# Optimization experiments

Measured on AMD Instinct MI355X. Metric: run time of the kernel, lower is better.

Reference implementation:

```python
import jax, jax.numpy as jnp
import numpy as np

B, S, D, H = 2, 2048, 2048, 16
HD = D // H  # head_dim = 128
ROPE_BASE = 10000.0


def _rope_tables(seq_len, head_dim, base, dtype):
    inv_freq = 1.0 / (base ** (jnp.arange(0, head_dim, 2, dtype=jnp.float32) / head_dim))
    t = jnp.arange(seq_len, dtype=jnp.float32)
    freqs = jnp.einsum('s,d->sd', t, inv_freq)           # [S, HD/2]
    emb = jnp.concatenate([freqs, freqs], axis=-1)        # [S, HD]
    return jnp.cos(emb).astype(dtype), jnp.sin(emb).astype(dtype)


def _rotate_half(x):
    half = x.shape[-1] // 2
    return jnp.concatenate([-x[..., half:], x[..., :half]], axis=-1)


def setup_inputs() -> dict:
    key = jax.random.key(0)
    kx, kq, kk, kv, ko = jax.random.split(key, 5)
    std = 0.02
    return {
        'x': jax.random.normal(kx, (B, S, D), dtype=jnp.float32),
        'Wq': jax.random.normal(kq, (D, D), dtype=jnp.float32) * std,
        'Wk': jax.random.normal(kk, (D, D), dtype=jnp.float32) * std,
        'Wv': jax.random.normal(kv, (D, D), dtype=jnp.float32) * std,
        'Wo': jax.random.normal(ko, (D, D), dtype=jnp.float32) * std,
    }


def reference(x, Wq, Wk, Wv, Wo):
    b, s, d = x.shape
    scale = HD ** -0.5
    # projections (nn.Linear: x @ W.T), split heads -> [b, h, s, hd]
    q = (x @ Wq.T).reshape(b, s, H, HD).transpose(0, 2, 1, 3)
    k = (x @ Wk.T).reshape(b, s, H, HD).transpose(0, 2, 1, 3)
    v = (x @ Wv.T).reshape(b, s, H, HD).transpose(0, 2, 1, 3)
    cos, sin = _rope_tables(s, HD, ROPE_BASE, x.dtype)    # [s, hd]
    q = q * cos + _rotate_half(q) * sin
    k = k * cos + _rotate_half(k) * sin
    scores = jnp.einsum('bhqd,bhkd->bhqk', q, k) * scale  # [b,h,s,s]
    causal = jnp.triu(jnp.ones((s, s), dtype=bool), k=1)
    scores = jnp.where(causal, jnp.float32(-jnp.inf).astype(scores.dtype), scores)
    attn = jax.nn.softmax(scores, axis=-1)
    out = jnp.einsum('bhqk,bhkd->bhqd', attn, v)
    out = out.transpose(0, 2, 1, 3).reshape(b, s, d)
    return out @ Wo.T
```

## Files before the change

### kernel.cpp

```cpp
#include <hip/hip_runtime.h>
#include <hip/hip_bf16.h>
#include <cstdint>
#include <cstddef>

#define B_ 2
#define S_ 2048
#define D_ 2048
#define H_ 16
#define HD_ 128

typedef __bf16 bf16_t;
typedef __bf16 bf16x8 __attribute__((ext_vector_type(8)));
typedef __bf16 bf16x4 __attribute__((ext_vector_type(4)));
typedef short s16x4 __attribute__((ext_vector_type(4)));
typedef float f32x4 __attribute__((ext_vector_type(4)));

__device__ __forceinline__ void async16(const bf16_t* g, bf16_t* l) {
    __builtin_amdgcn_global_load_lds(
        (const __attribute__((address_space(1))) unsigned int*)g,
        (__attribute__((address_space(3))) unsigned int*)l, 16, 0, 0);
}

__device__ __forceinline__ f32x4 mfma16x16x16_bf16(bf16x4 a, bf16x4 b, f32x4 c) {
#if __has_builtin(__builtin_amdgcn_mfma_f32_16x16x16_bf16)
    return __builtin_amdgcn_mfma_f32_16x16x16_bf16(a, b, c, 0, 0, 0);
#elif __has_builtin(__builtin_amdgcn_mfma_f32_16x16x16bf16_1k)
    return __builtin_amdgcn_mfma_f32_16x16x16bf16_1k(
        __builtin_bit_cast(s16x4, a), __builtin_bit_cast(s16x4, b), c, 0, 0, 0);
#else
    f32x4 d = c;
    asm("v_mfma_f32_16x16x16_bf16 %0, %1, %2, %0" : "+v"(d) : "v"(a), "v"(b));
    return d;
#endif
}

__global__ void f2b_multi(const float* __restrict__ x, const float* __restrict__ wq,
                          const float* __restrict__ wk, const float* __restrict__ wv,
                          const float* __restrict__ wo, bf16_t* __restrict__ xb,
                          bf16_t* __restrict__ wqb, bf16_t* __restrict__ wkb,
                          bf16_t* __restrict__ wvb, bf16_t* __restrict__ wob) {
    const float* in; bf16_t* out;
    switch (blockIdx.y) {
        case 0: in = x;            out = xb;            break;
        case 1: in = x + 4194304;  out = xb + 4194304;  break;
        case 2: in = wq;           out = wqb;           break;
        case 3: in = wk;           out = wkb;           break;
        case 4: in = wv;           out = wvb;           break;
        default: in = wo;          out = wob;           break;
    }
    int i = (blockIdx.x * blockDim.x + threadIdx.x) * 4;
    float4 v = *(const float4*)(in + i);
    bf16x4 o = { (bf16_t)v.x, (bf16_t)v.y, (bf16_t)v.z, (bf16_t)v.w };
    *(bf16x4*)(out + i) = o;
}

__global__ void rope_kernel(bf16_t* __restrict__ q, bf16_t* __restrict__ k) {
    int idx = blockIdx.x * blockDim.x + threadIdx.x;
    bf16_t* p = (blockIdx.y == 0) ? q : k;
    float sc = (blockIdx.y == 0) ? 0.08838834764831845f : 1.0f;
    int i0 = (idx & 7) * 8;
    int rest = idx >> 3;
    int h = rest & (H_ - 1);
    int row = rest >> 4;
    int s = row & (S_ - 1);
    size_t base = (size_t)row * D_ + (size_t)h * HD_ + i0;
    bf16x8 x0 = *(bf16x8*)(p + base);
    bf16x8 x1 = *(bf16x8*)(p + base + 64);
    bf16x8 o0, o1;
#pragma unroll
    for (int j = 0; j < 8; ++j) {
        float inv = __expf(-(float)(i0 + j) * 0.14391156831212787f);
        float ang = (float)s * inv;
        float sn, c;
        __sincosf(ang, &sn, &c);
        sn *= sc; c *= sc;
        float a = (float)x0[j], bb = (float)x1[j];
        o0[j] = (bf16_t)(a * c - bb * sn);
        o1[j] = (bf16_t)(bb * c + a * sn);
    }
    *(bf16x8*)(p + base) = o0;
    *(bf16x8*)(p + base + 64) = o1;
}

__global__ __launch_bounds__(256) void gemm_qkv(const bf16_t* __restrict__ A,
                                                const bf16_t* __restrict__ Wq,
                                                const bf16_t* __restrict__ Wk,
                                                const bf16_t* __restrict__ Wv,
                                                bf16_t* __restrict__ qb,
                                                bf16_t* __restrict__ kb,
                                                bf16_t* __restrict__ vtb) {
    __shared__ __align__(16) bf16_t As[128 * 32];
    __shared__ __align__(16) bf16_t Bs[128 * 32];
    const int K = D_;
    int t = threadIdx.x;
    int w = t >> 6, lane = t & 63, lo = lane & 15, hi = lane >> 4;
    int seg = blockIdx.x >> 4;
    int n0 = (blockIdx.x & 15) * 128;
    int m0 = blockIdx.y * 128;
    const bf16_t* Bt = (seg == 0) ? Wq : (seg == 1) ? Wk : Wv;
    int wm = (w & 1) * 64, wn = (w >> 1) * 64;
    f32x4 acc[4][4] = {};
    const bf16_t* ga = A + (size_t)(m0 + (t >> 2)) * K + (t & 3) * 8;
    const bf16_t* gb = Bt + (size_t)(n0 + (t >> 2)) * K + (t & 3) * 8;
    for (int k0 = 0; k0 < K; k0 += 32) {
        async16(ga + k0,                  As + t * 8);
        async16(ga + (size_t)64 * K + k0, As + 2048 + t * 8);
        async16(gb + k0,                  Bs + t * 8);
        async16(gb + (size_t)64 * K + k0, Bs + 2048 + t * 8);
        __syncthreads();
        bf16x8 af[4], bfr[4];
#pragma unroll
        for (int ms = 0; ms < 4; ++ms)
            af[ms] = *(const bf16x8*)(As + (wm + ms * 16 + lo) * 32 + hi * 8);
#pragma unroll
        for (int ns = 0; ns < 4; ++ns)
            bfr[ns] = *(const bf16x8*)(Bs + (wn + ns * 16 + lo) * 32 + hi * 8);
#pragma unroll
        for (int ms = 0; ms < 4; ++ms)
#pragma unroll
            for (int ns = 0; ns < 4; ++ns)
                acc[ms][ns] = __builtin_amdgcn_mfma_f32_16x16x32_bf16(af[ms], bfr[ns], acc[ms][ns], 0, 0, 0);
        __syncthreads();
    }
    if (seg < 2) {
        bf16_t* C = (seg == 0) ? qb : kb;
#pragma unroll
        for (int ms = 0; ms < 4; ++ms)
#pragma unroll
            for (int ns = 0; ns < 4; ++ns)
#pragma unroll
                for (int r = 0; r < 4; ++r)
                    C[(size_t)(m0 + wm + ms * 16 + hi * 4 + r) * D_ + n0 + wn + ns * 16 + lo] = (bf16_t)acc[ms][ns][r];
    } else {
#pragma unroll
        for (int ms = 0; ms < 4; ++ms) {
            int mrow = m0 + wm + ms * 16 + hi * 4;
            int bb = mrow >> 11, s = mrow & (S_ - 1);
#pragma unroll
            for (int ns = 0; ns < 4; ++ns) {
                int d = n0 + wn + ns * 16 + lo;
                bf16x4 pv = { (bf16_t)acc[ms][ns][0], (bf16_t)acc[ms][ns][1],
                              (bf16_t)acc[ms][ns][2], (bf16_t)acc[ms][ns][3] };
                *(bf16x4*)(vtb + (size_t)bb * D_ * S_ + (size_t)d * S_ + s) = pv;
            }
        }
    }
}

__global__ __launch_bounds__(256) void gemm_bt_f32(const bf16_t* __restrict__ A,
                                                   const bf16_t* __restrict__ Bt,
                                                   float* __restrict__ C,
                                                   int M, int N, int K) {
    __shared__ __align__(16) bf16_t As[128 * 32];
    __shared__ __align__(16) bf16_t Bs[128 * 32];
    int t = threadIdx.x;
    int w = t >> 6, lane = t & 63, lo = lane & 15, hi = lane >> 4;
    int m0 = blockIdx.y * 128, n0 = blockIdx.x * 128;
    int wm = (w & 1) * 64, wn = (w >> 1) * 64;
    f32x4 acc[4][4] = {};
    const bf16_t* ga = A + (size_t)(m0 + (t >> 2)) * K + (t & 3) * 8;
    const bf16_t* gb = Bt + (size_t)(n0 + (t >> 2)) * K + (t & 3) * 8;
    for (int k0 = 0; k0 < K; k0 += 32) {
        async16(ga + k0,                  As + t * 8);
        async16(ga + (size_t)64 * K + k0, As + 2048 + t * 8);
        async16(gb + k0,                  Bs + t * 8);
        async16(gb + (size_t)64 * K + k0, Bs + 2048 + t * 8);
        __syncthreads();
        bf16x8 af[4], bfr[4];
#pragma unroll
        for (int ms = 0; ms < 4; ++ms)
            af[ms] = *(const bf16x8*)(As + (wm + ms * 16 + lo) * 32 + hi * 8);
#pragma unroll
        for (int ns = 0; ns < 4; ++ns)
            bfr[ns] = *(const bf16x8*)(Bs + (wn + ns * 16 + lo) * 32 + hi * 8);
#pragma unroll
        for (int ms = 0; ms < 4; ++ms)
#pragma unroll
            for (int ns = 0; ns < 4; ++ns)
                acc[ms][ns] = __builtin_amdgcn_mfma_f32_16x16x32_bf16(af[ms], bfr[ns], acc[ms][ns], 0, 0, 0);
        __syncthreads();
    }
#pragma unroll
    for (int ms = 0; ms < 4; ++ms)
#pragma unroll
        for (int ns = 0; ns < 4; ++ns)
#pragma unroll
            for (int r = 0; r < 4; ++r)
                C[(size_t)(m0 + wm + ms * 16 + hi * 4 + r) * N + n0 + wn + ns * 16 + lo] = acc[ms][ns][r];
}

__global__ __launch_bounds__(256) void attn_kernel(const bf16_t* __restrict__ q,
                                                   const bf16_t* __restrict__ k,
                                                   const bf16_t* __restrict__ vt,
                                                   bf16_t* __restrict__ o) {
    __shared__ __align__(16) bf16_t Ks[64 * 128];
    __shared__ __align__(16) bf16_t Vs[128 * 64];
    int t = threadIdx.x;
    int w = t >> 6, lane = t & 63, lo = lane & 15, hi = lane >> 4;
    int bx = blockIdx.x;
    int b = blockIdx.y >> 4, h = blockIdx.y & 15;
    const size_t head_off = (size_t)b * S_ * D_ + (size_t)h * HD_;
    const size_t vhead_off = ((size_t)b * D_ + (size_t)h * HD_) * S_;

#pragma unroll 1
    for (int pass = 0; pass < 2; ++pass) {
        int qt = pass ? (31 - bx) : bx;
        int q0 = qt * 64;
        int qg = q0 + w * 16 + lo;
        bf16x8 aq[4];
#pragma unroll
        for (int c = 0; c < 4; ++c)
            aq[c] = *(const bf16x8*)(q + head_off + (size_t)qg * D_ + c * 32 + hi * 8);

        float l_part = 0.f;
        f32x4 oacc[8] = {};
        int nkt = qt + 1;
        for (int kt = 0; kt < nkt; ++kt) {
            int k0 = kt * 64;
            __syncthreads();
#pragma unroll
            for (int i = 0; i < 4; ++i) {
                int chunk = w * 4 + i;
                int r = chunk * 4 + (lane >> 4);
                int lc = (lane & 15) ^ (r & 15);
                async16(k + head_off + (size_t)(k0 + r) * D_ + lc * 8,
                        Ks + chunk * 512 + lane * 8);
            }
#pragma unroll
            for (int i = 0; i < 4; ++i) {
                int chunk = w * 4 + i;
                int d = chunk * 8 + (lane >> 3);
                int lc = (lane & 7) ^ (d & 7);
                async16(vt + vhead_off + (size_t)d * S_ + k0 + lc * 8,
                        Vs + chunk * 512 + lane * 8);
            }
            __syncthreads();

            f32x4 sacc[4] = {};
#pragma unroll
            for (int c = 0; c < 4; ++c) {
#pragma unroll
                for (int nt = 0; nt < 4; ++nt) {
                    int row = nt * 16 + lo;
                    int pc = (c * 4 + hi) ^ lo;
                    bf16x8 ak = *(const bf16x8*)(Ks + row * 128 + pc * 8);
                    sacc[nt] = __builtin_amdgcn_mfma_f32_16x16x32_bf16(ak, aq[c], sacc[nt], 0, 0, 0);
                }
            }
            bool diag = (kt == qt);
            bf16x4 pf[4];
#pragma unroll
            for (int nt = 0; nt < 4; ++nt) {
#pragma unroll
                for (int r = 0; r < 4; ++r) {
                    float e = __expf(fminf(sacc[nt][r], 60.f));
                    if (diag) {
                        int kg = k0 + nt * 16 + hi * 4 + r;
                        if (kg > qg) e = 0.f;
                    }
                    l_part += e;
                    pf[nt][r] = (bf16_t)e;
                }
            }
#pragma unroll
            for (int nt = 0; nt < 4; ++nt) {
                int kkb = nt * 16 + hi * 4;
                int chunk8 = kkb >> 3, rem = kkb & 7;
#pragma unroll
                for (int dt = 0; dt < 8; ++dt) {
                    int d = dt * 16 + lo;
                    bf16x4 av = *(const bf16x4*)(Vs + d * 64 + (chunk8 ^ (d & 7)) * 8 + rem);
                    oacc[dt] = mfma16x16x16_bf16(av, pf[nt], oacc[dt]);
                }
            }
        }
        float l = l_part;
        l += __shfl_xor(l, 16);
        l += __shfl_xor(l, 32);
        float rl = 1.0f / l;
#pragma unroll
        for (int dt = 0; dt < 8; ++dt) {
            bf16x4 ov = { (bf16_t)(oacc[dt][0] * rl), (bf16_t)(oacc[dt][1] * rl),
                          (bf16_t)(oacc[dt][2] * rl), (bf16_t)(oacc[dt][3] * rl) };
            *(bf16x4*)(o + head_off + (size_t)qg * D_ + dt * 16 + hi * 4) = ov;
        }
    }
}

extern "C" void kernel_launch(void* const* d_in, const int* in_sizes, int n_in,
                              void* d_out, int out_size, void* d_ws, size_t ws_size,
                              hipStream_t stream) {
    (void)in_sizes; (void)n_in; (void)out_size; (void)ws_size;
    const float* x  = (const float*)d_in[0];
    const float* Wq = (const float*)d_in[1];
    const float* Wk = (const float*)d_in[2];
    const float* Wv = (const float*)d_in[3];
    const float* Wo = (const float*)d_in[4];
    char* ws = (char*)d_ws;
    bf16_t* xb  = (bf16_t*)(ws);
    bf16_t* Wqb = (bf16_t*)(ws + 16777216);
    bf16_t* Wkb = (bf16_t*)(ws + 25165824);
    bf16_t* Wvb = (bf16_t*)(ws + 33554432);
    bf16_t* Wob = (bf16_t*)(ws + 41943040);
    bf16_t* qb  = (bf16_t*)(ws + 50331648);
    bf16_t* kb  = (bf16_t*)(ws + 67108864);
    bf16_t* vtb = (bf16_t*)(ws + 83886080);
    bf16_t* ob  = (bf16_t*)(ws + 100663296);
    float* out = (float*)d_out;

    f2b_multi<<<dim3(4096, 6), 256, 0, stream>>>(x, Wq, Wk, Wv, Wo, xb, Wqb, Wkb, Wvb, Wob);

    gemm_qkv<<<dim3(48, 32), 256, 0, stream>>>(xb, Wqb, Wkb, Wvb, qb, kb, vtb);

    rope_kernel<<<dim3((B_ * S_ * H_ * 8) / 256, 2), 256, 0, stream>>>(qb, kb);

    attn_kernel<<<dim3(16, B_ * H_), 256, 0, stream>>>(qb, kb, vtb, ob);

    gemm_bt_f32<<<dim3(D_ / 128, (B_ * S_) / 128), 256, 0, stream>>>(ob, Wob, out, B_ * S_, D_, D_);
}
```

Measured before the change: 407.9 us.

## Fuse RoPE into QKV GEMM epilogue and enlarge attention key tiles to 128

A precomputed cos/sin table replaces the standalone RoPE kernel. Rotation now happens in the QKV GEMM epilogue, with wave N-columns remapped so each lane holds both rotation halves. The softmax scale is folded into the Wq bf16 conversion. The attention kernel processes 128-key tiles with larger shared-memory buffers and skips waves fully past the causal boundary, trading an extra memory pass for higher LDS use and possible occupancy loss.

```diff
diff --git a/kernel.cpp b/kernel.cpp
--- a/kernel.cpp
+++ b/kernel.cpp
@@ -40,52 +40,36 @@
                           bf16_t* __restrict__ wqb, bf16_t* __restrict__ wkb,
                           bf16_t* __restrict__ wvb, bf16_t* __restrict__ wob) {
     const float* in; bf16_t* out;
+    float sc = 1.0f;
     switch (blockIdx.y) {
         case 0: in = x;            out = xb;            break;
         case 1: in = x + 4194304;  out = xb + 4194304;  break;
-        case 2: in = wq;           out = wqb;           break;
+        case 2: in = wq;           out = wqb; sc = 0.08838834764831845f; break;
         case 3: in = wk;           out = wkb;           break;
         case 4: in = wv;           out = wvb;           break;
         default: in = wo;          out = wob;           break;
     }
     int i = (blockIdx.x * blockDim.x + threadIdx.x) * 4;
     float4 v = *(const float4*)(in + i);
-    bf16x4 o = { (bf16_t)v.x, (bf16_t)v.y, (bf16_t)v.z, (bf16_t)v.w };
+    bf16x4 o = { (bf16_t)(v.x * sc), (bf16_t)(v.y * sc), (bf16_t)(v.z * sc), (bf16_t)(v.w * sc) };
     *(bf16x4*)(out + i) = o;
 }
 
-__global__ void rope_kernel(bf16_t* __restrict__ q, bf16_t* __restrict__ k) {
+__global__ void rope_tab(float2* __restrict__ tab) {
     int idx = blockIdx.x * blockDim.x + threadIdx.x;
-    bf16_t* p = (blockIdx.y == 0) ? q : k;
-    float sc = (blockIdx.y == 0) ? 0.08838834764831845f : 1.0f;
-    int i0 = (idx & 7) * 8;
-    int rest = idx >> 3;
-    int h = rest & (H_ - 1);
-    int row = rest >> 4;
-    int s = row & (S_ - 1);
-    size_t base = (size_t)row * D_ + (size_t)h * HD_ + i0;
-    bf16x8 x0 = *(bf16x8*)(p + base);
-    bf16x8 x1 = *(bf16x8*)(p + base + 64);
-    bf16x8 o0, o1;
-#pragma unroll
-    for (int j = 0; j < 8; ++j) {
-        float inv = __expf(-(float)(i0 + j) * 0.14391156831212787f);
-        float ang = (float)s * inv;
-        float sn, c;
-        __sincosf(ang, &sn, &c);
-        sn *= sc; c *= sc;
-        float a = (float)x0[j], bb = (float)x1[j];
-        o0[j] = (bf16_t)(a * c - bb * sn);
-        o1[j] = (bf16_t)(bb * c + a * sn);
-    }
-    *(bf16x8*)(p + base) = o0;
-    *(bf16x8*)(p + base + 64) = o1;
+    int s = idx >> 6, j = idx & 63;
+    float inv = __expf(-(float)j * 0.14391156831212787f);
+    float ang = (float)s * inv;
+    float sn, c;
+    __sincosf(ang, &sn, &c);
+    tab[idx] = make_float2(c, sn);
 }
 
 __global__ __launch_bounds__(256) void gemm_qkv(const bf16_t* __restrict__ A,
                                                 const bf16_t* __restrict__ Wq,
                                                 const bf16_t* __restrict__ Wk,
                                                 const bf16_t* __restrict__ Wv,
+                                                const float2* __restrict__ tab,
                                                 bf16_t* __restrict__ qb,
                                                 bf16_t* __restrict__ kb,
                                                 bf16_t* __restrict__ vtb) {
@@ -98,7 +82,7 @@
     int n0 = (blockIdx.x & 15) * 128;
     int m0 = blockIdx.y * 128;
     const bf16_t* Bt = (seg == 0) ? Wq : (seg == 1) ? Wk : Wv;
-    int wm = (w & 1) * 64, wn = (w >> 1) * 64;
+    int wm = (w & 1) * 64, W = (w >> 1);
     f32x4 acc[4][4] = {};
     const bf16_t* ga = A + (size_t)(m0 + (t >> 2)) * K + (t & 3) * 8;
     const bf16_t* gb = Bt + (size_t)(n0 + (t >> 2)) * K + (t & 3) * 8;
@@ -114,7 +98,7 @@
             af[ms] = *(const bf16x8*)(As + (wm + ms * 16 + lo) * 32 + hi * 8);
 #pragma unroll
         for (int ns = 0; ns < 4; ++ns)
-            bfr[ns] = *(const bf16x8*)(Bs + (wn + ns * 16 + lo) * 32 + hi * 8);
+            bfr[ns] = *(const bf16x8*)(Bs + (W * 16 + ns * 32 + lo) * 32 + hi * 8);
 #pragma unroll
         for (int ms = 0; ms < 4; ++ms)
 #pragma unroll
@@ -124,13 +108,25 @@
     }
     if (seg < 2) {
         bf16_t* C = (seg == 0) ? qb : kb;
-#pragma unroll
-        for (int ms = 0; ms < 4; ++ms)
-#pragma unroll
-            for (int ns = 0; ns < 4; ++ns)
-#pragma unroll
-                for (int r = 0; r < 4; ++r)
-                    C[(size_t)(m0 + wm + ms * 16 + hi * 4 + r) * D_ + n0 + wn + ns * 16 + lo] = (bf16_t)acc[ms][ns][r];
+        int j0 = W * 16 + lo;
+#pragma unroll
+        for (int ms = 0; ms < 4; ++ms) {
+            int mbase = m0 + wm + ms * 16 + hi * 4;
+#pragma unroll
+            for (int r = 0; r < 4; ++r) {
+                int m = mbase + r;
+                int s = m & (S_ - 1);
+                const float2* trow = tab + s * 64;
+#pragma unroll
+                for (int ns = 0; ns < 2; ++ns) {
+                    int j = j0 + ns * 32;
+                    float2 cs = trow[j];
+                    float v0 = acc[ms][ns][r], v1 = acc[ms][ns + 2][r];
+                    C[(size_t)m * D_ + n0 + j]      = (bf16_t)(v0 * cs.x - v1 * cs.y);
+                    C[(size_t)m * D_ + n0 + j + 64] = (bf16_t)(v1 * cs.x + v0 * cs.y);
+                }
+            }
+        }
     } else {
 #pragma unroll
         for (int ms = 0; ms < 4; ++ms) {
@@ -138,7 +134,7 @@
             int bb = mrow >> 11, s = mrow & (S_ - 1);
 #pragma unroll
             for (int ns = 0; ns < 4; ++ns) {
-                int d = n0 + wn + ns * 16 + lo;
+                int d = n0 + W * 16 + ns * 32 + lo;
                 bf16x4 pv = { (bf16_t)acc[ms][ns][0], (bf16_t)acc[ms][ns][1],
                               (bf16_t)acc[ms][ns][2], (bf16_t)acc[ms][ns][3] };
                 *(bf16x4*)(vtb + (size_t)bb * D_ * S_ + (size_t)d * S_ + s) = pv;
@@ -193,8 +189,8 @@
                                                    const bf16_t* __restrict__ k,
                                                    const bf16_t* __restrict__ vt,
                                                    bf16_t* __restrict__ o) {
-    __shared__ __align__(16) bf16_t Ks[64 * 128];
-    __shared__ __align__(16) bf16_t Vs[128 * 64];
+    __shared__ __align__(16) bf16_t Ks[128 * 128];
+    __shared__ __align__(16) bf16_t Vs[128 * 128];
     int t = threadIdx.x;
     int w = t >> 6, lane = t & 63, lo = lane & 15, hi = lane >> 4;
     int bx = blockIdx.x;
@@ -214,63 +210,65 @@
 
         float l_part = 0.f;
         f32x4 oacc[8] = {};
-        int nkt = qt + 1;
+        int nkt = (qt >> 1) + 1;
         for (int kt = 0; kt < nkt; ++kt) {
-            int k0 = kt * 64;
+            int k0 = kt * 128;
             __syncthreads();
 #pragma unroll
-            for (int i = 0; i < 4; ++i) {
-                int chunk = w * 4 + i;
+            for (int i = 0; i < 8; ++i) {
+                int chunk = w * 8 + i;
                 int r = chunk * 4 + (lane >> 4);
                 int lc = (lane & 15) ^ (r & 15);
                 async16(k + head_off + (size_t)(k0 + r) * D_ + lc * 8,
                         Ks + chunk * 512 + lane * 8);
             }
 #pragma unroll
-            for (int i = 0; i < 4; ++i) {
-                int chunk = w * 4 + i;
-                int d = chunk * 8 + (lane >> 3);
-                int lc = (lane & 7) ^ (d & 7);
+            for (int i = 0; i < 8; ++i) {
+                int chunk = w * 8 + i;
+                int d = chunk * 4 + (lane >> 4);
+                int lc = (lane & 15) ^ (d & 15);
                 async16(vt + vhead_off + (size_t)d * S_ + k0 + lc * 8,
                         Vs + chunk * 512 + lane * 8);
             }
             __syncthreads();
 
-            f32x4 sacc[4] = {};
-#pragma unroll
-            for (int c = 0; c < 4; ++c) {
-#pragma unroll
-                for (int nt = 0; nt < 4; ++nt) {
-                    int row = nt * 16 + lo;
-                    int pc = (c * 4 + hi) ^ lo;
-                    bf16x8 ak = *(const bf16x8*)(Ks + row * 128 + pc * 8);
-                    sacc[nt] = __builtin_amdgcn_mfma_f32_16x16x32_bf16(ak, aq[c], sacc[nt], 0, 0, 0);
+            if (k0 <= q0 + w * 16 + 15) {
+                f32x4 sacc[8] = {};
+#pragma unroll
+                for (int c = 0; c < 4; ++c) {
+#pragma unroll
+                    for (int nt = 0; nt < 8; ++nt) {
+                        int row = nt * 16 + lo;
+                        int pc = (c * 4 + hi) ^ lo;
+                        bf16x8 ak = *(const bf16x8*)(Ks + row * 128 + pc * 8);
+                        sacc[nt] = __builtin_amdgcn_mfma_f32_16x16x32_bf16(ak, aq[c], sacc[nt], 0, 0, 0);
+                    }
                 }
-            }
-            bool diag = (kt == qt);
-            bf16x4 pf[4];
-#pragma unroll
-            for (int nt = 0; nt < 4; ++nt) {
-#pragma unroll
-                for (int r = 0; r < 4; ++r) {
-                    float e = __expf(fminf(sacc[nt][r], 60.f));
-                    if (diag) {
-                        int kg = k0 + nt * 16 + hi * 4 + r;
-                        if (kg > qg) e = 0.f;
+                bool diag = (k0 + 127 > q0 + w * 16);
+                bf16x4 pf[8];
+#pragma unroll
+                for (int nt = 0; nt < 8; ++nt) {
+#pragma unroll
+                    for (int r = 0; r < 4; ++r) {
+                        float e = __expf(fminf(sacc[nt][r], 60.f));
+                        if (diag) {
+                            int kg = k0 + nt * 16 + hi * 4 + r;
+                            if (kg > qg) e = 0.f;
+                        }
+                        l_part += e;
+                        pf[nt][r] = (bf16_t)e;
                     }
-                    l_part += e;
-                    pf[nt][r] = (bf16_t)e;
                 }
-            }
-#pragma unroll
-            for (int nt = 0; nt < 4; ++nt) {
-                int kkb = nt * 16 + hi * 4;
-                int chunk8 = kkb >> 3, rem = kkb & 7;
-#pragma unroll
-                for (int dt = 0; dt < 8; ++dt) {
-                    int d = dt * 16 + lo;
-                    bf16x4 av = *(const bf16x4*)(Vs + d * 64 + (chunk8 ^ (d & 7)) * 8 + rem);
-                    oacc[dt] = mfma16x16x16_bf16(av, pf[nt], oacc[dt]);
+#pragma unroll
+                for (int nt = 0; nt < 8; ++nt) {
+                    int kkb = nt * 16 + hi * 4;
+                    int c16 = kkb >> 3, rem = kkb & 7;
+#pragma unroll
+                    for (int dt = 0; dt < 8; ++dt) {
+                        int d = dt * 16 + lo;
+                        bf16x4 av = *(const bf16x4*)(Vs + d * 128 + (c16 ^ (d & 15)) * 8 + rem);
+                        oacc[dt] = mfma16x16x16_bf16(av, pf[nt], oacc[dt]);
+                    }
                 }
             }
         }
@@ -306,13 +304,13 @@
     bf16_t* kb  = (bf16_t*)(ws + 67108864);
     bf16_t* vtb = (bf16_t*)(ws + 83886080);
     bf16_t* ob  = (bf16_t*)(ws + 100663296);
+    float2* tab = (float2*)(ws + 100663296);
     float* out = (float*)d_out;
 
+    rope_tab<<<512, 256, 0, stream>>>(tab);
     f2b_multi<<<dim3(4096, 6), 256, 0, stream>>>(x, Wq, Wk, Wv, Wo, xb, Wqb, Wkb, Wvb, Wob);
 
-    gemm_qkv<<<dim3(48, 32), 256, 0, stream>>>(xb, Wqb, Wkb, Wvb, qb, kb, vtb);
-
-    rope_kernel<<<dim3((B_ * S_ * H_ * 8) / 256, 2), 256, 0, stream>>>(qb, kb);
+    gemm_qkv<<<dim3(48, 32), 256, 0, stream>>>(xb, Wqb, Wkb, Wvb, tab, qb, kb, vtb);
 
     attn_kernel<<<dim3(16, B_ * H_), 256, 0, stream>>>(qb, kb, vtb, ob);
 
```

Result: slower. 419.0 us (+2.7%).

## Widen GEMM K-tile to 64 with swizzled LDS and use 128-key attention tiles

Applied to the files above, without the earlier changes.

Both GEMM kernels now stage a 64-wide K slice per iteration with an XOR-swizzled LDS layout, which halves the number of barrier pairs per tile and is meant to reduce LDS bank conflicts. The attention kernel loads 128 keys per iteration instead of 64, and each wave skips tiles that lie entirely above its causal boundary. The softmax scale is folded into the Wq conversion instead of the RoPE kernel. These changes raise LDS use and register pressure (attention LDS doubles to 64KB), which can lower occupancy.

```diff
diff --git a/kernel.cpp b/kernel.cpp
--- a/kernel.cpp
+++ b/kernel.cpp
@@ -40,24 +40,24 @@
                           bf16_t* __restrict__ wqb, bf16_t* __restrict__ wkb,
                           bf16_t* __restrict__ wvb, bf16_t* __restrict__ wob) {
     const float* in; bf16_t* out;
+    float sc = 1.0f;
     switch (blockIdx.y) {
         case 0: in = x;            out = xb;            break;
         case 1: in = x + 4194304;  out = xb + 4194304;  break;
-        case 2: in = wq;           out = wqb;           break;
+        case 2: in = wq;           out = wqb; sc = 0.08838834764831845f; break;
         case 3: in = wk;           out = wkb;           break;
         case 4: in = wv;           out = wvb;           break;
         default: in = wo;          out = wob;           break;
     }
     int i = (blockIdx.x * blockDim.x + threadIdx.x) * 4;
     float4 v = *(const float4*)(in + i);
-    bf16x4 o = { (bf16_t)v.x, (bf16_t)v.y, (bf16_t)v.z, (bf16_t)v.w };
+    bf16x4 o = { (bf16_t)(v.x * sc), (bf16_t)(v.y * sc), (bf16_t)(v.z * sc), (bf16_t)(v.w * sc) };
     *(bf16x4*)(out + i) = o;
 }
 
 __global__ void rope_kernel(bf16_t* __restrict__ q, bf16_t* __restrict__ k) {
     int idx = blockIdx.x * blockDim.x + threadIdx.x;
     bf16_t* p = (blockIdx.y == 0) ? q : k;
-    float sc = (blockIdx.y == 0) ? 0.08838834764831845f : 1.0f;
     int i0 = (idx & 7) * 8;
     int rest = idx >> 3;
     int h = rest & (H_ - 1);
@@ -73,7 +73,6 @@
         float ang = (float)s * inv;
         float sn, c;
         __sincosf(ang, &sn, &c);
-        sn *= sc; c *= sc;
         float a = (float)x0[j], bb = (float)x1[j];
         o0[j] = (bf16_t)(a * c - bb * sn);
         o1[j] = (bf16_t)(bb * c + a * sn);
@@ -81,6 +80,7 @@
     *(bf16x8*)(p + base) = o0;
     *(bf16x8*)(p + base + 64) = o1;
 }
+
 
 __global__ __launch_bounds__(256) void gemm_qkv(const bf16_t* __restrict__ A,
                                                 const bf16_t* __restrict__ Wq,
@@ -89,8 +89,8 @@
                                                 bf16_t* __restrict__ qb,
                                                 bf16_t* __restrict__ kb,
                                                 bf16_t* __restrict__ vtb) {
-    __shared__ __align__(16) bf16_t As[128 * 32];
-    __shared__ __align__(16) bf16_t Bs[128 * 32];
+    __shared__ __align__(16) bf16_t As[128 * 64];
+    __shared__ __align__(16) bf16_t Bs[128 * 64];
     const int K = D_;
     int t = threadIdx.x;
     int w = t >> 6, lane = t & 63, lo = lane & 15, hi = lane >> 4;
@@ -100,26 +100,35 @@
     const bf16_t* Bt = (seg == 0) ? Wq : (seg == 1) ? Wk : Wv;
     int wm = (w & 1) * 64, wn = (w >> 1) * 64;
     f32x4 acc[4][4] = {};
-    const bf16_t* ga = A + (size_t)(m0 + (t >> 2)) * K + (t & 3) * 8;
-    const bf16_t* gb = Bt + (size_t)(n0 + (t >> 2)) * K + (t & 3) * 8;
-    for (int k0 = 0; k0 < K; k0 += 32) {
-        async16(ga + k0,                  As + t * 8);
-        async16(ga + (size_t)64 * K + k0, As + 2048 + t * 8);
-        async16(gb + k0,                  Bs + t * 8);
-        async16(gb + (size_t)64 * K + k0, Bs + 2048 + t * 8);
+    int srow = w * 32 + (lane >> 3);
+    int scol = ((lane & 7) ^ (lane >> 3)) * 8;
+    const bf16_t* gA = A  + (size_t)(m0 + srow) * K + scol;
+    const bf16_t* gB = Bt + (size_t)(n0 + srow) * K + scol;
+    bf16_t* lA = As + w * 2048 + lane * 8;
+    bf16_t* lB = Bs + w * 2048 + lane * 8;
+    for (int k0 = 0; k0 < K; k0 += 64) {
+#pragma unroll
+        for (int i = 0; i < 4; ++i) {
+            async16(gA + (size_t)(i * 8) * K + k0, lA + i * 512);
+            async16(gB + (size_t)(i * 8) * K + k0, lB + i * 512);
+        }
         __syncthreads();
-        bf16x8 af[4], bfr[4];
-#pragma unroll
-        for (int ms = 0; ms < 4; ++ms)
-            af[ms] = *(const bf16x8*)(As + (wm + ms * 16 + lo) * 32 + hi * 8);
-#pragma unroll
-        for (int ns = 0; ns < 4; ++ns)
-            bfr[ns] = *(const bf16x8*)(Bs + (wn + ns * 16 + lo) * 32 + hi * 8);
-#pragma unroll
-        for (int ms = 0; ms < 4; ++ms)
+#pragma unroll
+        for (int kk = 0; kk < 2; ++kk) {
+            bf16x8 af[4], bfr[4];
+            int pc = (kk * 4 + hi) ^ (lo & 7);
+#pragma unroll
+            for (int ms = 0; ms < 4; ++ms)
+                af[ms] = *(const bf16x8*)(As + (wm + ms * 16 + lo) * 64 + pc * 8);
 #pragma unroll
             for (int ns = 0; ns < 4; ++ns)
-                acc[ms][ns] = __builtin_amdgcn_mfma_f32_16x16x32_bf16(af[ms], bfr[ns], acc[ms][ns], 0, 0, 0);
+                bfr[ns] = *(const bf16x8*)(Bs + (wn + ns * 16 + lo) * 64 + pc * 8);
+#pragma unroll
+            for (int ms = 0; ms < 4; ++ms)
+#pragma unroll
+                for (int ns = 0; ns < 4; ++ns)
+                    acc[ms][ns] = __builtin_amdgcn_mfma_f32_16x16x32_bf16(af[ms], bfr[ns], acc[ms][ns], 0, 0, 0);
+        }
         __syncthreads();
     }
     if (seg < 2) {
@@ -151,33 +160,42 @@
                                                    const bf16_t* __restrict__ Bt,
                                                    float* __restrict__ C,
                                                    int M, int N, int K) {
-    __shared__ __align__(16) bf16_t As[128 * 32];
-    __shared__ __align__(16) bf16_t Bs[128 * 32];
+    __shared__ __align__(16) bf16_t As[128 * 64];
+    __shared__ __align__(16) bf16_t Bs[128 * 64];
     int t = threadIdx.x;
     int w = t >> 6, lane = t & 63, lo = lane & 15, hi = lane >> 4;
     int m0 = blockIdx.y * 128, n0 = blockIdx.x * 128;
     int wm = (w & 1) * 64, wn = (w >> 1) * 64;
     f32x4 acc[4][4] = {};
-    const bf16_t* ga = A + (size_t)(m0 + (t >> 2)) * K + (t & 3) * 8;
-    const bf16_t* gb = Bt + (size_t)(n0 + (t >> 2)) * K + (t & 3) * 8;
-    for (int k0 = 0; k0 < K; k0 += 32) {
-        async16(ga + k0,                  As + t * 8);
-        async16(ga + (size_t)64 * K + k0, As + 2048 + t * 8);
-        async16(gb + k0,                  Bs + t * 8);
-        async16(gb + (size_t)64 * K + k0, Bs + 2048 + t * 8);
+    int srow = w * 32 + (lane >> 3);
+    int scol = ((lane & 7) ^ (lane >> 3)) * 8;
+    const bf16_t* gA = A  + (size_t)(m0 + srow) * K + scol;
+    const bf16_t* gB = Bt + (size_t)(n0 + srow) * K + scol;
+    bf16_t* lA = As + w * 2048 + lane * 8;
+    bf16_t* lB = Bs + w * 2048 + lane * 8;
+    for (int k0 = 0; k0 < K; k0 += 64) {
+#pragma unroll
+        for (int i = 0; i < 4; ++i) {
+            async16(gA + (size_t)(i * 8) * K + k0, lA + i * 512);
+            async16(gB + (size_t)(i * 8) * K + k0, lB + i * 512);
+        }
         __syncthreads();
-        bf16x8 af[4], bfr[4];
-#pragma unroll
-        for (int ms = 0; ms < 4; ++ms)
-            af[ms] = *(const bf16x8*)(As + (wm + ms * 16 + lo) * 32 + hi * 8);
-#pragma unroll
-        for (int ns = 0; ns < 4; ++ns)
-            bfr[ns] = *(const bf16x8*)(Bs + (wn + ns * 16 + lo) * 32 + hi * 8);
-#pragma unroll
-        for (int ms = 0; ms < 4; ++ms)
+#pragma unroll
+        for (int kk = 0; kk < 2; ++kk) {
+            bf16x8 af[4], bfr[4];
+            int pc = (kk * 4 + hi) ^ (lo & 7);
+#pragma unroll
+            for (int ms = 0; ms < 4; ++ms)
+                af[ms] = *(const bf16x8*)(As + (wm + ms * 16 + lo) * 64 + pc * 8);
 #pragma unroll
             for (int ns = 0; ns < 4; ++ns)
-                acc[ms][ns] = __builtin_amdgcn_mfma_f32_16x16x32_bf16(af[ms], bfr[ns], acc[ms][ns], 0, 0, 0);
+                bfr[ns] = *(const bf16x8*)(Bs + (wn + ns * 16 + lo) * 64 + pc * 8);
+#pragma unroll
+            for (int ms = 0; ms < 4; ++ms)
+#pragma unroll
+                for (int ns = 0; ns < 4; ++ns)
+                    acc[ms][ns] = __builtin_amdgcn_mfma_f32_16x16x32_bf16(af[ms], bfr[ns], acc[ms][ns], 0, 0, 0);
+        }
         __syncthreads();
     }
 #pragma unroll
@@ -193,8 +211,8 @@
                                                    const bf16_t* __restrict__ k,
                                                    const bf16_t* __restrict__ vt,
                                                    bf16_t* __restrict__ o) {
-    __shared__ __align__(16) bf16_t Ks[64 * 128];
-    __shared__ __align__(16) bf16_t Vs[128 * 64];
+    __shared__ __align__(16) bf16_t Ks[128 * 128];
+    __shared__ __align__(16) bf16_t Vs[128 * 128];
     int t = threadIdx.x;
     int w = t >> 6, lane = t & 63, lo = lane & 15, hi = lane >> 4;
     int bx = blockIdx.x;
@@ -214,63 +232,65 @@
 
         float l_part = 0.f;
         f32x4 oacc[8] = {};
-        int nkt = qt + 1;
+        int nkt = (qt >> 1) + 1;
         for (int kt = 0; kt < nkt; ++kt) {
-            int k0 = kt * 64;
+            int k0 = kt * 128;
             __syncthreads();
 #pragma unroll
-            for (int i = 0; i < 4; ++i) {
-                int chunk = w * 4 + i;
+            for (int i = 0; i < 8; ++i) {
+                int chunk = w * 8 + i;
                 int r = chunk * 4 + (lane >> 4);
                 int lc = (lane & 15) ^ (r & 15);
                 async16(k + head_off + (size_t)(k0 + r) * D_ + lc * 8,
                         Ks + chunk * 512 + lane * 8);
             }
 #pragma unroll
-            for (int i = 0; i < 4; ++i) {
-                int chunk = w * 4 + i;
-                int d = chunk * 8 + (lane >> 3);
-                int lc = (lane & 7) ^ (d & 7);
+            for (int i = 0; i < 8; ++i) {
+                int chunk = w * 8 + i;
+                int d = chunk * 4 + (lane >> 4);
+                int lc = (lane & 15) ^ (d & 15);
                 async16(vt + vhead_off + (size_t)d * S_ + k0 + lc * 8,
                         Vs + chunk * 512 + lane * 8);
             }
             __syncthreads();
 
-            f32x4 sacc[4] = {};
-#pragma unroll
-            for (int c = 0; c < 4; ++c) {
-#pragma unroll
-                for (int nt = 0; nt < 4; ++nt) {
-                    int row = nt * 16 + lo;
-                    int pc = (c * 4 + hi) ^ lo;
-                    bf16x8 ak = *(const bf16x8*)(Ks + row * 128 + pc * 8);
-                    sacc[nt] = __builtin_amdgcn_mfma_f32_16x16x32_bf16(ak, aq[c], sacc[nt], 0, 0, 0);
+            if (k0 <= q0 + w * 16 + 15) {
+                f32x4 sacc[8] = {};
+#pragma unroll
+                for (int c = 0; c < 4; ++c) {
+#pragma unroll
+                    for (int nt = 0; nt < 8; ++nt) {
+                        int row = nt * 16 + lo;
+                        int pc = (c * 4 + hi) ^ lo;
+                        bf16x8 ak = *(const bf16x8*)(Ks + row * 128 + pc * 8);
+                        sacc[nt] = __builtin_amdgcn_mfma_f32_16x16x32_bf16(ak, aq[c], sacc[nt], 0, 0, 0);
+                    }
                 }
-            }
-            bool diag = (kt == qt);
-            bf16x4 pf[4];
-#pragma unroll
-            for (int nt = 0; nt < 4; ++nt) {
-#pragma unroll
-                for (int r = 0; r < 4; ++r) {
-                    float e = __expf(fminf(sacc[nt][r], 60.f));
-                    if (diag) {
-                        int kg = k0 + nt * 16 + hi * 4 + r;
-                        if (kg > qg) e = 0.f;
+                bool diag = (k0 + 127 > q0 + w * 16);
+                bf16x4 pf[8];
+#pragma unroll
+                for (int nt = 0; nt < 8; ++nt) {
+#pragma unroll
+                    for (int r = 0; r < 4; ++r) {
+                        float e = __expf(fminf(sacc[nt][r], 60.f));
+                        if (diag) {
+                            int kg = k0 + nt * 16 + hi * 4 + r;
+                            if (kg > qg) e = 0.f;
+                        }
+                        l_part += e;
+                        pf[nt][r] = (bf16_t)e;
                     }
-                    l_part += e;
-                    pf[nt][r] = (bf16_t)e;
                 }
-            }
-#pragma unroll
-            for (int nt = 0; nt < 4; ++nt) {
-                int kkb = nt * 16 + hi * 4;
-                int chunk8 = kkb >> 3, rem = kkb & 7;
-#pragma unroll
-                for (int dt = 0; dt < 8; ++dt) {
-                    int d = dt * 16 + lo;
-                    bf16x4 av = *(const bf16x4*)(Vs + d * 64 + (chunk8 ^ (d & 7)) * 8 + rem);
-                    oacc[dt] = mfma16x16x16_bf16(av, pf[nt], oacc[dt]);
+#pragma unroll
+                for (int nt = 0; nt < 8; ++nt) {
+                    int kkb = nt * 16 + hi * 4;
+                    int c16 = kkb >> 3, rem = kkb & 7;
+#pragma unroll
+                    for (int dt = 0; dt < 8; ++dt) {
+                        int d = dt * 16 + lo;
+                        bf16x4 av = *(const bf16x4*)(Vs + d * 128 + (c16 ^ (d & 15)) * 8 + rem);
+                        oacc[dt] = mfma16x16x16_bf16(av, pf[nt], oacc[dt]);
+                    }
                 }
             }
         }
```

New measurement: 382.2 us. 1.07x faster.
